# Kernel optimization log

Measured on AMD Instinct MI355X. Metric: run time of the kernel, lower is better.

Reference implementation:

```python
import jax, jax.numpy as jnp
import numpy as np

N = 100000      # nodes
E = 1600000     # edges (avg degree 16)
F = 64          # input node features
H = 128         # hidden channels
R = 20          # num relations (edge types)
G = 64          # graphs in batch
C = 10          # num classes
L = 2           # num RGCN layers
EPS = 1e-5      # BatchNorm eps


def setup_inputs() -> dict:
    key = jax.random.key(0)
    ks = jax.random.split(key, 14)
    s = 0.05
    return {
        "x": jax.random.normal(ks[0], (N, F), jnp.float32),
        "edge_index": jax.random.randint(ks[1], (2, E), 0, N, jnp.int32),
        "edge_type": jax.random.randint(ks[2], (E,), 0, R, jnp.int32),
        "batch": jnp.sort(jax.random.randint(ks[3], (N,), 0, G, jnp.int32)),
        # params
        "w_in": jax.random.normal(ks[4], (F, H), jnp.float32) * s,
        "b_in": jnp.zeros((H,), jnp.float32),
        "rel_w": jax.random.normal(ks[5], (L, R, H, H), jnp.float32) * s,
        "root_w": jax.random.normal(ks[6], (L, H, H), jnp.float32) * s,
        "conv_b": jnp.zeros((L, H), jnp.float32),
        "bn_g": jnp.ones((L, H), jnp.float32),
        "bn_b": jnp.zeros((L, H), jnp.float32),
        "w_out": jax.random.normal(ks[7], (H, C), jnp.float32) * s,
        "b_out": jnp.zeros((C,), jnp.float32),
    }


def reference(x, edge_index, edge_type, batch, w_in, b_in, rel_w, root_w,
              conv_b, bn_g, bn_b, w_out, b_out):
    # input MLP (dropout is identity in eval)
    h = jax.nn.relu(x @ w_in + b_in)

    src, dst = edge_index[0], edge_index[1]
    # per-(dst,relation) in-degree for RGCNConv mean aggregation
    comb = dst * R + edge_type                             # [E]
    cnt = jax.ops.segment_sum(jnp.ones((E,), jnp.float32), comb,
                              num_segments=N * R)
    edge_norm = (1.0 / jnp.maximum(cnt, 1.0))[comb]        # [E]

    for l in range(L):
        msg = h[src] * edge_norm[:, None]                  # [E, H] normalized source feats
        out = h @ root_w[l] + conv_b[l]                    # root/self transform + bias
        for r in range(R):
            mask = (edge_type == r).astype(h.dtype)        # [E]
            agg = jax.ops.segment_sum(msg * mask[:, None], dst,
                                      num_segments=N)      # [N, H] per-relation mean
            out = out + agg @ rel_w[l, r]
        # BatchNorm1d (training-mode batch statistics over nodes)
        mu = out.mean(axis=0)
        var = out.var(axis=0)
        out = (out - mu) * jax.lax.rsqrt(var + EPS) * bn_g[l] + bn_b[l]
        h = jax.nn.relu(out)                               # dropout = identity (eval)

    # global mean pool over graphs
    sums = jax.ops.segment_sum(h, batch, num_segments=G)   # [G, H]
    counts = jax.ops.segment_sum(jnp.ones((N,), h.dtype), batch, num_segments=G)
    pooled = sums / jnp.maximum(counts, 1.0)[:, None]

    logits = pooled @ w_out + b_out                        # [G, C]
    return jax.nn.sigmoid(logits)
```

## Files before the change

kernel.cpp:

```cpp
#include <hip/hip_runtime.h>

#define N_NODES 100000
#define E_EDGES 1600000
#define F_IN    64
#define H_DIM   128
#define R_REL   20
#define G_GRAPHS 64
#define C_CLASSES 10
#define L_LAYERS 2
#define BN_EPS  1e-5f
#define RN      (R_REL * N_NODES)

typedef unsigned short u16;
typedef unsigned int   u32;
typedef __attribute__((ext_vector_type(8))) short short8;
typedef __attribute__((ext_vector_type(4))) float f32x4;

static __device__ __forceinline__ float bf2f(u16 u) {
    u32 b = ((u32)u) << 16;
    return __builtin_bit_cast(float, b);
}
static __device__ __forceinline__ u16 f2bf(float f) {
    u32 x = __builtin_bit_cast(u32, f);
    u32 r = x + 0x7fff + ((x >> 16) & 1);
    return (u16)(r >> 16);
}


__global__ void count_kernel(const int* __restrict__ ei, const int* __restrict__ et,
                             int* __restrict__ hist, int* __restrict__ erank) {
    for (int e = blockIdx.x * blockDim.x + threadIdx.x; e < E_EDGES;
         e += gridDim.x * blockDim.x) {
        int t = et[e];
        int d = ei[E_EDGES + e];
        erank[e] = atomicAdd(&hist[t * N_NODES + d], 1);
    }
}

__global__ void scan1_kernel(const int* __restrict__ in, int* __restrict__ out,
                             int* __restrict__ part, int n) {
    __shared__ int s[256];
    int t = threadIdx.x;
    int base = blockIdx.x * 1024;
    int v[4]; int sum = 0;
#pragma unroll
    for (int j = 0; j < 4; ++j) {
        int i = base + t * 4 + j;
        v[j] = (i < n) ? in[i] : 0;
        sum += v[j];
    }
    s[t] = sum;
    __syncthreads();
    for (int off = 1; off < 256; off <<= 1) {
        int x = (t >= off) ? s[t - off] : 0;
        __syncthreads();
        s[t] += x;
        __syncthreads();
    }
    if (t == 255) part[blockIdx.x] = s[255];
    int run = s[t] - sum;
#pragma unroll
    for (int j = 0; j < 4; ++j) {
        int i = base + t * 4 + j;
        if (i < n) out[i] = run;
        run += v[j];
    }
}

__global__ void scan2_kernel(int* __restrict__ part, int nb) {
    __shared__ int s[256];
    int t = threadIdx.x;
    int loc[8]; int sum = 0;
#pragma unroll
    for (int j = 0; j < 8; ++j) {
        int i = t * 8 + j;
        loc[j] = (i < nb) ? part[i] : 0;
        sum += loc[j];
    }
    s[t] = sum;
    __syncthreads();
    for (int off = 1; off < 256; off <<= 1) {
        int x = (t >= off) ? s[t - off] : 0;
        __syncthreads();
        s[t] += x;
        __syncthreads();
    }
    int run = s[t] - sum;
#pragma unroll
    for (int j = 0; j < 8; ++j) {
        int i = t * 8 + j;
        if (i < nb) part[i] = run;
        run += loc[j];
    }
}

__global__ void scan3_kernel(int* __restrict__ out, const int* __restrict__ part, int n) {
    for (int i = blockIdx.x * blockDim.x + threadIdx.x; i < n;
         i += gridDim.x * blockDim.x)
        out[i] += part[i >> 10];
    if (blockIdx.x == 0 && threadIdx.x == 0) out[n] = E_EDGES;
}

__global__ void bucket_kernel(const int* __restrict__ ei, const int* __restrict__ et,
                              const int* __restrict__ off2, const int* __restrict__ erank,
                              int2* __restrict__ epair) {
    for (int e = blockIdx.x * blockDim.x + threadIdx.x; e < E_EDGES;
         e += gridDim.x * blockDim.x) {
        int t = et[e];
        int s = ei[e];
        int d = ei[E_EDGES + e];
        epair[off2[t * N_NODES + d] + erank[e]] = make_int2(s, d);
    }
}

template<int K>
__global__ void pack_w(const float* __restrict__ W, u16* __restrict__ Wp) {
    const float* w = W + (size_t)blockIdx.x * K * H_DIM;
    u16* p = Wp + (size_t)blockIdx.x * K * H_DIM;
    for (int o = threadIdx.x; o < K * H_DIM; o += blockDim.x) {
        int j  = o & 7;
        int l  = (o >> 3) & 63;
        int ct = (o >> 9) & 7;
        int kt = o >> 12;
        int k  = kt * 32 + (l >> 4) * 8 + j;
        int n  = ct * 16 + (l & 15);
        p[o] = f2bf(w[(size_t)k * H_DIM + n]);
    }
}

__global__ void cvt_bf16_kernel(const float* __restrict__ in, u16* __restrict__ out, int n4) {
    for (int i = blockIdx.x * blockDim.x + threadIdx.x; i < n4;
         i += gridDim.x * blockDim.x) {
        float4 v = ((const float4*)in)[i];
        ushort4 o;
        o.x = f2bf(v.x); o.y = f2bf(v.y); o.z = f2bf(v.z); o.w = f2bf(v.w);
        ((ushort4*)out)[i] = o;
    }
}

template<int K, bool RELU, bool HASBIAS, bool OUTBF16>
__global__ __launch_bounds__(256)
void mfma_dense(const u16* __restrict__ A, const u16* __restrict__ Wp,
                const float* __restrict__ bias, void* __restrict__ OutV, int M) {
    constexpr int CH = K / 8;
    __shared__ u16 Ws[K * H_DIM];
    __shared__ u16 As[64 * H_DIM];

    for (int o = threadIdx.x; o < K * H_DIM / 8; o += 256)
        ((short8*)Ws)[o] = ((const short8*)Wp)[o];

    const int lane = threadIdx.x & 63;
    const int wave = threadIdx.x >> 6;
    const int l15  = lane & 15;
    const int kgrp = lane >> 4;
    const int arow = wave * 16 + l15;

    for (int tb = blockIdx.x * 64; tb < M; tb += gridDim.x * 64) {
        __syncthreads();
        for (int o = threadIdx.x; o < 64 * CH; o += 256) {
            int row = o / CH, cc = o % CH;
            int grow = tb + row;
            short8 v = {0,0,0,0,0,0,0,0};
            if (grow < M) v = *(const short8*)&A[(size_t)grow * K + cc * 8];
            *(short8*)&As[row * K + ((cc ^ (row & 7)) * 8)] = v;
        }
        __syncthreads();

        f32x4 acc[8];
#pragma unroll
        for (int i = 0; i < 8; ++i) {
            acc[i][0] = 0.f; acc[i][1] = 0.f; acc[i][2] = 0.f; acc[i][3] = 0.f;
        }
#pragma unroll
        for (int kt = 0; kt < K / 32; ++kt) {
            short8 af = *(const short8*)&As[arow * K + (((kt * 4 + kgrp) ^ (arow & 7)) * 8)];
#pragma unroll
            for (int ct = 0; ct < 8; ++ct) {
                short8 bf = *(const short8*)&Ws[(((kt * 8 + ct) * 64) + lane) * 8];
                acc[ct] = __builtin_amdgcn_mfma_f32_16x16x32_bf16(af, bf, acc[ct], 0, 0, 0);
            }
        }

        if (OUTBF16) {
            __syncthreads();
#pragma unroll
            for (int ct = 0; ct < 8; ++ct) {
#pragma unroll
                for (int r = 0; r < 4; ++r) {
                    int row = wave * 16 + kgrp * 4 + r;
                    int col = ct * 16 + l15;
                    float v = acc[ct][r];
                    if (HASBIAS) v += bias[col];
                    if (RELU)    v = fmaxf(v, 0.f);
                    As[row * H_DIM + ((((col >> 3) ^ (row & 7)) << 3) | (col & 7))] = f2bf(v);
                }
            }
            __syncthreads();
            u16* Out = (u16*)OutV;
            for (int o = threadIdx.x; o < 64 * 16; o += 256) {
                int row = o >> 4, cc = o & 15;
                int grow = tb + row;
                if (grow < M)
                    *(short8*)&Out[(size_t)grow * H_DIM + cc * 8] =
                        *(const short8*)&As[row * H_DIM + ((cc ^ (row & 7)) << 3)];
            }
        } else {
            float* Out = (float*)OutV;
#pragma unroll
            for (int ct = 0; ct < 8; ++ct) {
#pragma unroll
                for (int r = 0; r < 4; ++r) {
                    int grow = tb + wave * 16 + kgrp * 4 + r;
                    if (grow < M) {
                        float v = acc[ct][r];
                        if (HASBIAS) v += bias[ct * 16 + l15];
                        if (RELU)    v = fmaxf(v, 0.f);
                        Out[(size_t)grow * H_DIM + ct * 16 + l15] = v;
                    }
                }
            }
        }
    }
}

__global__ __launch_bounds__(256, 4)
void rgcn_conv(const u16* __restrict__ h, const u16* __restrict__ Wrel,
               const u16* __restrict__ Wroot, const float* __restrict__ bias,
               const int2* __restrict__ epair, const int* __restrict__ off2,
               float* __restrict__ outb, float* __restrict__ bn_sums) {
    __shared__ int offs[R_REL][65];
    __shared__ u16 Abf[64 * H_DIM];
    __shared__ float bnS[H_DIM], bnSS[H_DIM];

    const int d0 = blockIdx.x * 64;
    for (int i = threadIdx.x; i < R_REL * 65; i += 256) {
        int r = i / 65, j = i % 65;
        offs[r][j] = off2[r * N_NODES + min(d0 + j, N_NODES)];
    }
    if (threadIdx.x < H_DIM) { bnS[threadIdx.x] = 0.f; bnSS[threadIdx.x] = 0.f; }

    const int lane = threadIdx.x & 63;
    const int wv   = threadIdx.x >> 6;
    const int l15  = lane & 15;
    const int kgrp = lane >> 4;
    const int arow = wv * 16 + l15;
    const u32* h2  = (const u32*)h;
    u32* Ab32 = (u32*)Abf;

    f32x4 acc[8];
#pragma unroll
    for (int i = 0; i < 8; ++i) {
        acc[i][0] = 0.f; acc[i][1] = 0.f; acc[i][2] = 0.f; acc[i][3] = 0.f;
    }

    auto flushrow = [&](int dcur, int cnt, float f0, float f1) {
        float nm = 1.0f / (float)cnt;
        int dr = dcur - d0;
        u32 pk = (u32)f2bf(f0 * nm) | ((u32)f2bf(f1 * nm) << 16);
        Ab32[dr * 64 + ((((lane >> 2) ^ (dr & 7)) << 2) | (lane & 3))] = pk;
    };

    __syncthreads();

    for (int r = 0; r < R_REL; ++r) {
        const int estart = __builtin_amdgcn_readfirstlane(offs[r][wv * 16]);
        const int eend   = __builtin_amdgcn_readfirstlane(offs[r][wv * 16 + 16]);
        if (eend <= estart) continue;

#pragma unroll
        for (int i = 0; i < 16; ++i)
            Ab32[(wv * 16 + i) * 64 + lane] = 0u;

        {
            const int last = eend - 1;
            int ss[16], dd[16];
            u32 rv[16];
#pragma unroll
            for (int j = 0; j < 16; ++j) {
                int2 pr = epair[min(estart + j, last)];
                ss[j] = pr.x; dd[j] = pr.y;
            }
#pragma unroll
            for (int j = 0; j < 16; ++j)
                rv[j] = h2[(size_t)ss[j] * 64 + lane];

            int dcur = -1, cnt = 0;
            float f0 = 0.f, f1 = 0.f;
#pragma unroll
            for (int j = 0; j < 16; ++j) {
                if (estart + j < eend) {
                    if (dd[j] != dcur) {
                        if (dcur >= 0) flushrow(dcur, cnt, f0, f1);
                        dcur = dd[j]; f0 = 0.f; f1 = 0.f; cnt = 0;
                    }
                    f0 += bf2f((u16)(rv[j] & 0xffff));
                    f1 += bf2f((u16)(rv[j] >> 16));
                    cnt++;
                }
            }
            for (int e = estart + 16; e < eend; e += 16) {
                int ss2[16], dd2[16];
                u32 rv2[16];
#pragma unroll
                for (int j = 0; j < 16; ++j) {
                    int2 pr = epair[min(e + j, last)];
                    ss2[j] = pr.x; dd2[j] = pr.y;
                }
#pragma unroll
                for (int j = 0; j < 16; ++j)
                    rv2[j] = h2[(size_t)ss2[j] * 64 + lane];
#pragma unroll
                for (int j = 0; j < 16; ++j) {
                    if (e + j < eend) {
                        if (dd2[j] != dcur) {
                            if (dcur >= 0) flushrow(dcur, cnt, f0, f1);
                            dcur = dd2[j]; f0 = 0.f; f1 = 0.f; cnt = 0;
                        }
                        f0 += bf2f((u16)(rv2[j] & 0xffff));
                        f1 += bf2f((u16)(rv2[j] >> 16));
                        cnt++;
                    }
                }
            }
            if (dcur >= 0) flushrow(dcur, cnt, f0, f1);
        }

        const u16* Wr = Wrel + (size_t)r * H_DIM * H_DIM;
#pragma unroll
        for (int kt = 0; kt < 4; ++kt) {
            short8 af = *(const short8*)&Abf[arow * H_DIM + (((kt * 4 + kgrp) ^ (arow & 7)) * 8)];
#pragma unroll
            for (int ct = 0; ct < 8; ++ct) {
                short8 bf = *(const short8*)&Wr[(((kt * 8 + ct) * 64) + lane) * 8];
                acc[ct] = __builtin_amdgcn_mfma_f32_16x16x32_bf16(af, bf, acc[ct], 0, 0, 0);
            }
        }
    }

    {
        const int hrow = min(d0 + arow, N_NODES - 1);
#pragma unroll
        for (int kt = 0; kt < 4; ++kt) {
            short8 af = *(const short8*)&h[(size_t)hrow * H_DIM + kt * 32 + kgrp * 8];
#pragma unroll
            for (int ct = 0; ct < 8; ++ct) {
                short8 bf = *(const short8*)&Wroot[(((kt * 8 + ct) * 64) + lane) * 8];
                acc[ct] = __builtin_amdgcn_mfma_f32_16x16x32_bf16(af, bf, acc[ct], 0, 0, 0);
            }
        }
    }

#pragma unroll
    for (int ct = 0; ct < 8; ++ct) {
        float bv = bias[ct * 16 + l15];
        float sl = 0.f, sq = 0.f;
#pragma unroll
        for (int rr = 0; rr < 4; ++rr) {
            int grow = d0 + wv * 16 + kgrp * 4 + rr;
            if (grow < N_NODES) {
                float v = acc[ct][rr] + bv;
                outb[(size_t)grow * H_DIM + ct * 16 + l15] = v;
                sl += v;
                sq += v * v;
            }
        }
        sl += __shfl_xor(sl, 16); sl += __shfl_xor(sl, 32);
        sq += __shfl_xor(sq, 16); sq += __shfl_xor(sq, 32);
        if (kgrp == 0) {
            atomicAdd(&bnS[ct * 16 + l15], sl);
            atomicAdd(&bnSS[ct * 16 + l15], sq);
        }
    }
    __syncthreads();
    if (threadIdx.x < H_DIM) {
        atomicAdd(&bn_sums[threadIdx.x], bnS[threadIdx.x]);
        atomicAdd(&bn_sums[H_DIM + threadIdx.x], bnSS[threadIdx.x]);
    }
}

__global__ void bn_apply(const float* __restrict__ X, const float* __restrict__ sums,
                         const float* __restrict__ gg, const float* __restrict__ bb,
                         u16* __restrict__ Hout) {
    __shared__ float sc[H_DIM], sh[H_DIM];
    if (threadIdx.x < H_DIM) {
        float mean = sums[threadIdx.x] * (1.0f / N_NODES);
        float var  = sums[H_DIM + threadIdx.x] * (1.0f / N_NODES) - mean * mean;
        float inv  = rsqrtf(var + BN_EPS) * gg[threadIdx.x];
        sc[threadIdx.x] = inv;
        sh[threadIdx.x] = bb[threadIdx.x] - mean * inv;
    }
    __syncthreads();
    int total = N_NODES * (H_DIM / 4);
    for (int idx = blockIdx.x * 256 + threadIdx.x; idx < total; idx += gridDim.x * 256) {
        float4 v = ((const float4*)X)[idx];
        int c = (idx & 31) << 2;
        ushort4 o;
        o.x = f2bf(fmaxf(v.x * sc[c + 0] + sh[c + 0], 0.f));
        o.y = f2bf(fmaxf(v.y * sc[c + 1] + sh[c + 1], 0.f));
        o.z = f2bf(fmaxf(v.z * sc[c + 2] + sh[c + 2], 0.f));
        o.w = f2bf(fmaxf(v.w * sc[c + 3] + sh[c + 3], 0.f));
        ((ushort4*)Hout)[idx] = o;
    }
}

__global__ void pool_kernel(const u16* __restrict__ Hf, const int* __restrict__ batch,
                            float* __restrict__ pool, float* __restrict__ pcnt) {
    int col  = threadIdx.x & 127;
    int half = threadIdx.x >> 7;
    int chunk = (N_NODES + gridDim.x - 1) / gridDim.x;
    int start = blockIdx.x * chunk;
    int end   = min(N_NODES, start + chunk);
    int curg = -1;
    float acc = 0.f, c = 0.f;
    for (int row = start + half; row < end; row += 2) {
        int g = batch[row];
        if (g != curg) {
            if (curg >= 0) {
                atomicAdd(&pool[curg * H_DIM + col], acc);
                if (col == 0) atomicAdd(&pcnt[curg], c);
            }
            curg = g; acc = 0.f; c = 0.f;
        }
        acc += bf2f(Hf[(size_t)row * H_DIM + col]);
        c += 1.f;
    }
    if (curg >= 0) {
        atomicAdd(&pool[curg * H_DIM + col], acc);
        if (col == 0) atomicAdd(&pcnt[curg], c);
    }
}

__global__ void logits_kernel(const float* __restrict__ pool, const float* __restrict__ pcnt,
                              const float* __restrict__ w_out, const float* __restrict__ b_out,
                              float* __restrict__ out) {
    int g = blockIdx.x;
    __shared__ float p[H_DIM];
    float cnt = fmaxf(pcnt[g], 1.0f);
    p[threadIdx.x] = pool[g * H_DIM + threadIdx.x] / cnt;
    __syncthreads();
    if (threadIdx.x < C_CLASSES) {
        float acc = b_out[threadIdx.x];
        for (int k = 0; k < H_DIM; ++k)
            acc += p[k] * w_out[k * C_CLASSES + threadIdx.x];
        out[g * C_CLASSES + threadIdx.x] = 1.0f / (1.0f + expf(-acc));
    }
}

static inline size_t align256(size_t x) { return (x + 255) & ~(size_t)255; }

extern "C" void kernel_launch(void* const* d_in, const int* in_sizes, int n_in,
                              void* d_out, int out_size, void* d_ws, size_t ws_size,
                              hipStream_t stream) {
    const float* x      = (const float*)d_in[0];
    const int*   ei     = (const int*)d_in[1];
    const int*   et     = (const int*)d_in[2];
    const int*   batch  = (const int*)d_in[3];
    const float* w_in   = (const float*)d_in[4];
    const float* b_in   = (const float*)d_in[5];
    const float* rel_w  = (const float*)d_in[6];
    const float* root_w = (const float*)d_in[7];
    const float* conv_b = (const float*)d_in[8];
    const float* bn_g   = (const float*)d_in[9];
    const float* bn_b   = (const float*)d_in[10];
    const float* w_out  = (const float*)d_in[11];
    const float* b_out  = (const float*)d_in[12];
    float* out = (float*)d_out;

    char* ws = (char*)d_ws;
    size_t off = 0;
    u16*   h_bf  = (u16*)(ws + off);  off += align256((size_t)N_NODES * H_DIM * 2);
    float* outb  = (float*)(ws + off); off += align256((size_t)N_NODES * H_DIM * 4);
    u16*   x_bf  = (u16*)(ws + off);  off += align256((size_t)N_NODES * F_IN * 2);
    int*   off2  = (int*)(ws + off);  off += align256((size_t)(RN + 1) * 4 + 256);
    int*   hist  = (int*)(ws + off);  off += align256((size_t)RN * 4);
    int*   erank = (int*)(ws + off);  off += align256((size_t)E_EDGES * 4);
    int2*  e_pair = (int2*)(ws + off); off += align256((size_t)E_EDGES * 8 + 256);
    u16*   wp_in   = (u16*)(ws + off); off += align256((size_t)F_IN * H_DIM * 2);
    u16*   wp_root = (u16*)(ws + off); off += align256((size_t)L_LAYERS * H_DIM * H_DIM * 2);
    u16*   wp_rel  = (u16*)(ws + off); off += align256((size_t)L_LAYERS * R_REL * H_DIM * H_DIM * 2);
    int*   scan_part  = (int*)(ws + off); off += align256(2048 * 4);
    float* bn_sums    = (float*)(ws + off); off += align256(2 * H_DIM * 4);
    float* pool       = (float*)(ws + off); off += align256((size_t)G_GRAPHS * H_DIM * 4);
    float* pcnt       = (float*)(ws + off); off += 256;

    hipMemsetAsync(hist, 0, (size_t)RN * 4, stream);
    count_kernel<<<1024, 256, 0, stream>>>(ei, et, hist, erank);
    const int NB = (RN + 1023) / 1024;
    scan1_kernel<<<NB, 256, 0, stream>>>(hist, off2, scan_part, RN);
    scan2_kernel<<<1, 256, 0, stream>>>(scan_part, NB);
    scan3_kernel<<<2048, 256, 0, stream>>>(off2, scan_part, RN);
    bucket_kernel<<<2048, 256, 0, stream>>>(ei, et, off2, erank, e_pair);

    cvt_bf16_kernel<<<2048, 256, 0, stream>>>(x, x_bf, N_NODES * F_IN / 4);
    pack_w<F_IN><<<1, 256, 0, stream>>>(w_in, wp_in);
    pack_w<H_DIM><<<L_LAYERS, 256, 0, stream>>>(root_w, wp_root);
    pack_w<H_DIM><<<L_LAYERS * R_REL, 256, 0, stream>>>(rel_w, wp_rel);

    mfma_dense<F_IN, true, true, true><<<dim3(640), 256, 0, stream>>>(
        x_bf, wp_in, b_in, h_bf, N_NODES);

    const int CONV_BLOCKS = (N_NODES + 63) / 64;
    for (int l = 0; l < L_LAYERS; ++l) {
        hipMemsetAsync(bn_sums, 0, 2 * H_DIM * 4, stream);
        rgcn_conv<<<dim3(CONV_BLOCKS), 256, 0, stream>>>(
            h_bf, wp_rel + (size_t)l * R_REL * H_DIM * H_DIM,
            wp_root + (size_t)l * H_DIM * H_DIM, conv_b + (size_t)l * H_DIM,
            e_pair, off2, outb, bn_sums);
        bn_apply<<<2048, 256, 0, stream>>>(outb, bn_sums,
                                           bn_g + (size_t)l * H_DIM,
                                           bn_b + (size_t)l * H_DIM, h_bf);
    }

    hipMemsetAsync(pool, 0, (size_t)G_GRAPHS * H_DIM * 4, stream);
    hipMemsetAsync(pcnt, 0, 256, stream);
    pool_kernel<<<512, 256, 0, stream>>>(h_bf, batch, pool, pcnt);
    logits_kernel<<<G_GRAPHS, 128, 0, stream>>>(pool, pcnt, w_out, b_out, out);
}
```

Before: 732.7 us.

## Shrink RGCN conv tiles to 32 rows and fuse input conversion and weight packing

The RGCN conv kernel now uses 128-thread blocks that each cover 32 destination nodes instead of 64, with launch bounds raised to 8 blocks per SM. Halving the tile raises occupancy and balances the irregular per-node edge work better, in exchange for more blocks and more global BN atomics. The fp32-to-bf16 conversion of x is folded into the input dense kernel, and the weight-packing launches are merged into one kernel. All workspace zeroing is merged into a single memset, with separate BN accumulators per layer. Together these remove several launches and an intermediate buffer round trip.

After: 746.2 us. No clear change (+1.8%).

```diff
diff --git a/kernel.cpp b/kernel.cpp
--- a/kernel.cpp
+++ b/kernel.cpp
@@ -113,10 +113,16 @@
     }
 }
 
-template<int K>
-__global__ void pack_w(const float* __restrict__ W, u16* __restrict__ Wp) {
-    const float* w = W + (size_t)blockIdx.x * K * H_DIM;
-    u16* p = Wp + (size_t)blockIdx.x * K * H_DIM;
+__global__ void pack_all(const float* __restrict__ w_in, const float* __restrict__ root_w,
+                         const float* __restrict__ rel_w, u16* __restrict__ wp_in,
+                         u16* __restrict__ wp_root, u16* __restrict__ wp_rel) {
+    int b = blockIdx.x;
+    const float* w; u16* p; int K;
+    if (b == 0)      { w = w_in;  p = wp_in;  K = F_IN; }
+    else if (b <= 2) { w = root_w + (size_t)(b - 1) * H_DIM * H_DIM;
+                       p = wp_root + (size_t)(b - 1) * H_DIM * H_DIM; K = H_DIM; }
+    else             { w = rel_w + (size_t)(b - 3) * H_DIM * H_DIM;
+                       p = wp_rel + (size_t)(b - 3) * H_DIM * H_DIM; K = H_DIM; }
     for (int o = threadIdx.x; o < K * H_DIM; o += blockDim.x) {
         int j  = o & 7;
         int l  = (o >> 3) & 63;
@@ -128,19 +134,9 @@
     }
 }
 
-__global__ void cvt_bf16_kernel(const float* __restrict__ in, u16* __restrict__ out, int n4) {
-    for (int i = blockIdx.x * blockDim.x + threadIdx.x; i < n4;
-         i += gridDim.x * blockDim.x) {
-        float4 v = ((const float4*)in)[i];
-        ushort4 o;
-        o.x = f2bf(v.x); o.y = f2bf(v.y); o.z = f2bf(v.z); o.w = f2bf(v.w);
-        ((ushort4*)out)[i] = o;
-    }
-}
-
-template<int K, bool RELU, bool HASBIAS, bool OUTBF16>
+template<int K, bool INF32, bool RELU, bool HASBIAS, bool OUTBF16>
 __global__ __launch_bounds__(256)
-void mfma_dense(const u16* __restrict__ A, const u16* __restrict__ Wp,
+void mfma_dense(const void* __restrict__ Av, const u16* __restrict__ Wp,
                 const float* __restrict__ bias, void* __restrict__ OutV, int M) {
     constexpr int CH = K / 8;
     __shared__ u16 Ws[K * H_DIM];
@@ -161,7 +157,19 @@
             int row = o / CH, cc = o % CH;
             int grow = tb + row;
             short8 v = {0,0,0,0,0,0,0,0};
-            if (grow < M) v = *(const short8*)&A[(size_t)grow * K + cc * 8];
+            if (grow < M) {
+                if (INF32) {
+                    const float* xf = (const float*)Av;
+                    const float4* px = (const float4*)&xf[(size_t)grow * K + cc * 8];
+                    float4 a = px[0], b = px[1];
+                    v[0] = (short)f2bf(a.x); v[1] = (short)f2bf(a.y);
+                    v[2] = (short)f2bf(a.z); v[3] = (short)f2bf(a.w);
+                    v[4] = (short)f2bf(b.x); v[5] = (short)f2bf(b.y);
+                    v[6] = (short)f2bf(b.z); v[7] = (short)f2bf(b.w);
+                } else {
+                    v = *(const short8*)&((const u16*)Av)[(size_t)grow * K + cc * 8];
+                }
+            }
             *(short8*)&As[row * K + ((cc ^ (row & 7)) * 8)] = v;
         }
         __syncthreads();
@@ -223,21 +231,22 @@
     }
 }
 
-__global__ __launch_bounds__(256, 4)
+__global__ __launch_bounds__(128, 8)
 void rgcn_conv(const u16* __restrict__ h, const u16* __restrict__ Wrel,
                const u16* __restrict__ Wroot, const float* __restrict__ bias,
                const int2* __restrict__ epair, const int* __restrict__ off2,
                float* __restrict__ outb, float* __restrict__ bn_sums) {
-    __shared__ int offs[R_REL][65];
-    __shared__ u16 Abf[64 * H_DIM];
+    __shared__ int offs[R_REL][33];
+    __shared__ u16 Abf[32 * H_DIM];
     __shared__ float bnS[H_DIM], bnSS[H_DIM];
 
-    const int d0 = blockIdx.x * 64;
-    for (int i = threadIdx.x; i < R_REL * 65; i += 256) {
-        int r = i / 65, j = i % 65;
+    const int d0 = blockIdx.x * 32;
+    for (int i = threadIdx.x; i < R_REL * 33; i += 128) {
+        int r = i / 33, j = i % 33;
         offs[r][j] = off2[r * N_NODES + min(d0 + j, N_NODES)];
     }
-    if (threadIdx.x < H_DIM) { bnS[threadIdx.x] = 0.f; bnSS[threadIdx.x] = 0.f; }
+    bnS[threadIdx.x] = 0.f;
+    bnSS[threadIdx.x] = 0.f;
 
     const int lane = threadIdx.x & 63;
     const int wv   = threadIdx.x >> 6;
@@ -372,10 +381,8 @@
         }
     }
     __syncthreads();
-    if (threadIdx.x < H_DIM) {
-        atomicAdd(&bn_sums[threadIdx.x], bnS[threadIdx.x]);
-        atomicAdd(&bn_sums[H_DIM + threadIdx.x], bnSS[threadIdx.x]);
-    }
+    atomicAdd(&bn_sums[threadIdx.x], bnS[threadIdx.x]);
+    atomicAdd(&bn_sums[H_DIM + threadIdx.x], bnSS[threadIdx.x]);
 }
 
 __global__ void bn_apply(const float* __restrict__ X, const float* __restrict__ sums,
@@ -470,20 +477,23 @@
     size_t off = 0;
     u16*   h_bf  = (u16*)(ws + off);  off += align256((size_t)N_NODES * H_DIM * 2);
     float* outb  = (float*)(ws + off); off += align256((size_t)N_NODES * H_DIM * 4);
-    u16*   x_bf  = (u16*)(ws + off);  off += align256((size_t)N_NODES * F_IN * 2);
     int*   off2  = (int*)(ws + off);  off += align256((size_t)(RN + 1) * 4 + 256);
+    size_t zero_base = off;
     int*   hist  = (int*)(ws + off);  off += align256((size_t)RN * 4);
+    float* bnA   = (float*)(ws + off); off += align256(2 * H_DIM * 4);
+    float* bnB   = (float*)(ws + off); off += align256(2 * H_DIM * 4);
+    float* pool  = (float*)(ws + off); off += align256((size_t)G_GRAPHS * H_DIM * 4);
+    float* pcnt  = (float*)(ws + off); off += 256;
+    size_t zero_len = off - zero_base;
     int*   erank = (int*)(ws + off);  off += align256((size_t)E_EDGES * 4);
     int2*  e_pair = (int2*)(ws + off); off += align256((size_t)E_EDGES * 8 + 256);
     u16*   wp_in   = (u16*)(ws + off); off += align256((size_t)F_IN * H_DIM * 2);
     u16*   wp_root = (u16*)(ws + off); off += align256((size_t)L_LAYERS * H_DIM * H_DIM * 2);
     u16*   wp_rel  = (u16*)(ws + off); off += align256((size_t)L_LAYERS * R_REL * H_DIM * H_DIM * 2);
     int*   scan_part  = (int*)(ws + off); off += align256(2048 * 4);
-    float* bn_sums    = (float*)(ws + off); off += align256(2 * H_DIM * 4);
-    float* pool       = (float*)(ws + off); off += align256((size_t)G_GRAPHS * H_DIM * 4);
-    float* pcnt       = (float*)(ws + off); off += 256;
-
-    hipMemsetAsync(hist, 0, (size_t)RN * 4, stream);
+
+    hipMemsetAsync(ws + zero_base, 0, zero_len, stream);
+
     count_kernel<<<1024, 256, 0, stream>>>(ei, et, hist, erank);
     const int NB = (RN + 1023) / 1024;
     scan1_kernel<<<NB, 256, 0, stream>>>(hist, off2, scan_part, RN);
@@ -491,28 +501,24 @@
     scan3_kernel<<<2048, 256, 0, stream>>>(off2, scan_part, RN);
     bucket_kernel<<<2048, 256, 0, stream>>>(ei, et, off2, erank, e_pair);
 
-    cvt_bf16_kernel<<<2048, 256, 0, stream>>>(x, x_bf, N_NODES * F_IN / 4);
-    pack_w<F_IN><<<1, 256, 0, stream>>>(w_in, wp_in);
-    pack_w<H_DIM><<<L_LAYERS, 256, 0, stream>>>(root_w, wp_root);
-    pack_w<H_DIM><<<L_LAYERS * R_REL, 256, 0, stream>>>(rel_w, wp_rel);
-
-    mfma_dense<F_IN, true, true, true><<<dim3(640), 256, 0, stream>>>(
-        x_bf, wp_in, b_in, h_bf, N_NODES);
-
-    const int CONV_BLOCKS = (N_NODES + 63) / 64;
+    pack_all<<<3 + L_LAYERS * R_REL, 256, 0, stream>>>(w_in, root_w, rel_w,
+                                                       wp_in, wp_root, wp_rel);
+
+    mfma_dense<F_IN, true, true, true, true><<<dim3(640), 256, 0, stream>>>(
+        x, wp_in, b_in, h_bf, N_NODES);
+
+    const int CONV_BLOCKS = (N_NODES + 31) / 32;
     for (int l = 0; l < L_LAYERS; ++l) {
-        hipMemsetAsync(bn_sums, 0, 2 * H_DIM * 4, stream);
-        rgcn_conv<<<dim3(CONV_BLOCKS), 256, 0, stream>>>(
+        float* bns = (l == 0) ? bnA : bnB;
+        rgcn_conv<<<dim3(CONV_BLOCKS), 128, 0, stream>>>(
             h_bf, wp_rel + (size_t)l * R_REL * H_DIM * H_DIM,
             wp_root + (size_t)l * H_DIM * H_DIM, conv_b + (size_t)l * H_DIM,
-            e_pair, off2, outb, bn_sums);
-        bn_apply<<<2048, 256, 0, stream>>>(outb, bn_sums,
+            e_pair, off2, outb, bns);
+        bn_apply<<<2048, 256, 0, stream>>>(outb, bns,
                                            bn_g + (size_t)l * H_DIM,
                                            bn_b + (size_t)l * H_DIM, h_bf);
     }
 
-    hipMemsetAsync(pool, 0, (size_t)G_GRAPHS * H_DIM * 4, stream);
-    hipMemsetAsync(pcnt, 0, 256, stream);
     pool_kernel<<<512, 256, 0, stream>>>(h_bf, batch, pool, pcnt);
     logits_kernel<<<G_GRAPHS, 128, 0, stream>>>(pool, pcnt, w_out, b_out, out);
 }
```
